# Performance work log

Measured on AMD Instinct MI355X. Metric: run time of the kernel, lower is better.

## Reference

```python
import jax, jax.numpy as jnp
import numpy as np

K = 7  # kernel_size
C, H, W = 32, 192, 192


def setup_inputs() -> dict:
    key = jax.random.key(0)
    k1, k2, k3, k4 = jax.random.split(key, 4)
    x = jax.random.normal(k1, (C, H, W, 2), dtype=jnp.float32)
    # per-pixel kernel: (1, 1, K^2, H, W); original inits to ones/K^2, randomize for testing
    weight1 = jax.random.normal(k2, (1, 1, K * K, H, W), dtype=jnp.float32) / (K * K)
    # 1x1 conv c->c: weight (C_out, C_in) and bias (C,)
    conv_w = jax.random.normal(k3, (C, C), dtype=jnp.float32) / np.sqrt(C).astype(np.float32)
    conv_b = jax.random.normal(k4, (C,), dtype=jnp.float32) * 0.01
    return {"x": x, "weight1": weight1, "conv_w": conv_w, "conv_b": conv_b}


def conv_pixelwise(x, kernel):
    # x: (n, c, h, w); kernel: (1, 1, K^2, h, w)
    # Equivalent to: pad, unfold(K), reshape (n,c,K^2,h,w), * kernel, sum over K^2.
    # Implemented as a fused shift-multiply-accumulate over the K^2 fixed taps
    p = K // 2
    n, c, h, w = x.shape
    xp = jnp.pad(x, ((0, 0), (0, 0), (p, p), (p, p)))
    out = jnp.zeros_like(x)
    for i in range(K):
        for j in range(K):
            # F.unfold ordering: row-major over the KxK window -> index i*K + j
            out = out + xp[:, :, i:i + h, j:j + w] * kernel[:, :, i * K + j]
    return out


def reference(x, weight1, conv_w, conv_b):
    # x: (c, h, w, 2) -> (2, c, h, w)
    xi = jnp.transpose(x, (3, 0, 1, 2))
    xi = conv_pixelwise(xi, weight1)
    # 1x1 conv over channels + bias
    xi = jnp.einsum('nchw,oc->nohw', xi, conv_w) + conv_b[None, :, None, None]
    # back to (c, h, w, 2)
    return jnp.transpose(xi, (1, 2, 3, 0))
```

## Files before the change

### kernel.cpp

```cpp
#include <hip/hip_runtime.h>

#define C 32
#define H 192
#define W 192
#define HW (H*W)
#define NPIX (HW*2)
#define KK 7

__global__ __launch_bounds__(256) void k1_mix(
    const float* __restrict__ x, const float* __restrict__ cw, float* __restrict__ z)
{
    __shared__ float wl[256];
    const int b  = blockIdx.x;
    const int l  = (b & 7) * 72 + (b >> 3);
    const int hwblk = l >> 2;
    const int ob    = (l & 3) * 8;
    const int tid   = threadIdx.x;

    wl[tid] = cw[(ob + (tid & 7)) * C + (tid >> 3)];
    __syncthreads();

    const int hw = hwblk * 256 + tid;
    const float2* x2 = reinterpret_cast<const float2*>(x);
    float2 xv[C];
#pragma unroll
    for (int c = 0; c < C; ++c) xv[c] = x2[(size_t)c * HW + hw];

    float acc[8][2];
#pragma unroll
    for (int oo = 0; oo < 8; ++oo) { acc[oo][0] = 0.f; acc[oo][1] = 0.f; }

#pragma unroll
    for (int c = 0; c < C; ++c) {
        const float4 wa = *reinterpret_cast<const float4*>(&wl[c * 8]);
        const float4 wb = *reinterpret_cast<const float4*>(&wl[c * 8 + 4]);
        const float wt[8] = { wa.x, wa.y, wa.z, wa.w, wb.x, wb.y, wb.z, wb.w };
#pragma unroll
        for (int oo = 0; oo < 8; ++oo) {
            acc[oo][0] += wt[oo] * xv[c].x;
            acc[oo][1] += wt[oo] * xv[c].y;
        }
    }

    float* zp = z + (size_t)hw * 64 + ob * 2;
#pragma unroll
    for (int q = 0; q < 4; ++q) {
        float4 r = make_float4(acc[2*q][0], acc[2*q][1], acc[2*q+1][0], acc[2*q+1][1]);
        *reinterpret_cast<float4*>(zp + 4 * q) = r;
    }
}

#define K2_BLOCKS 1152
__global__ __launch_bounds__(256) void k2_conv(
    const float* __restrict__ z, const float* __restrict__ w1,
    const float* __restrict__ cb, float* __restrict__ out)
{
    __shared__ float tr[4][8 * 66];

    const int b  = blockIdx.x;
    const int l  = (b & 7) * (K2_BLOCKS / 8) + (b >> 3);
    const int h  = l / 6;
    const int wq = l % 6;
    const int tid  = threadIdx.x;
    const int wv   = __builtin_amdgcn_readfirstlane(tid >> 6);
    const int lane = tid & 63;
    const int w0   = wq * 32 + wv * 8;

    float acc[8];
#pragma unroll
    for (int p = 0; p < 8; ++p) acc[p] = 0.f;

    const bool wedge = (w0 == 0) || (w0 == W - 8);

#pragma unroll
    for (int i = 0; i < KK; ++i) {
        const int yy = h + i - 3;
        if (yy < 0 || yy >= H) continue;

        float zw[14];
        if (!wedge) {
            const float* p = z + ((size_t)yy * W + (w0 - 3)) * 64 + lane;
#pragma unroll
            for (int k = 0; k < 14; ++k) zw[k] = p[k * 64];
        } else {
            const float* p = z + (size_t)yy * (W * 64) + lane;
#pragma unroll
            for (int k = 0; k < 14; ++k) {
                const int cc  = w0 - 3 + k;
                const int ccl = cc < 0 ? 0 : (cc > W - 1 ? W - 1 : cc);
                const float v = p[ccl * 64];
                zw[k] = (cc == ccl) ? v : 0.f;
            }
        }

        const float* wp = w1 + (size_t)i * KK * HW + (size_t)h * W + w0;
#pragma unroll
        for (int j = 0; j < KK; ++j) {
#pragma unroll
            for (int px = 0; px < 8; ++px)
                acc[px] += wp[(size_t)j * HW + px] * zw[j + px];
        }
    }

    const float bias = cb[lane >> 1];
    float* trw = &tr[wv][0];
#pragma unroll
    for (int p = 0; p < 8; ++p) trw[p * 66 + lane] = acc[p] + bias;
    __syncthreads();

    const int o = lane >> 1, half = lane & 1;
    float v8[8];
#pragma unroll
    for (int m = 0; m < 8; ++m) {
        const int f = half * 8 + m;
        v8[m] = trw[(f >> 1) * 66 + o * 2 + (f & 1)];
    }
    float* obase = out + (size_t)o * NPIX + ((size_t)h * W + w0) * 2 + half * 8;
    *reinterpret_cast<float4*>(obase)     = make_float4(v8[0], v8[1], v8[2], v8[3]);
    *reinterpret_cast<float4*>(obase + 4) = make_float4(v8[4], v8[5], v8[6], v8[7]);
}

extern "C" void kernel_launch(void* const* d_in, const int* in_sizes, int n_in,
                              void* d_out, int out_size, void* d_ws, size_t ws_size,
                              hipStream_t stream) {
    const float* x  = (const float*)d_in[0];
    const float* w1 = (const float*)d_in[1];
    const float* cw = (const float*)d_in[2];
    const float* cb = (const float*)d_in[3];
    float* z   = (float*)d_ws;
    float* out = (float*)d_out;

    hipLaunchKernelGGL(k1_mix, dim3(576), dim3(256), 0, stream, x, cw, z);
    hipLaunchKernelGGL(k2_conv, dim3(K2_BLOCKS), dim3(256), 0, stream, z, w1, cb, out);
}
```

Baseline: 23.89 us.

## Retile pixelwise conv to two rows per thread with float4 channel loads

The conv kernel now gives each lane 4 channel values (float4) for one pixel across two output rows. Each loaded z row feeds both output rows, which cuts z reloads, and the LDS transpose and barrier before the output store are gone. The mix kernel is split into 4 output channels per block with twice as many blocks, which lowers register pressure. The cost is narrower 8-byte output stores, per-lane weight loads with masked taps, and an extra boundary-specialized template path.

```diff
diff --git a/kernel.cpp b/kernel.cpp
--- a/kernel.cpp
+++ b/kernel.cpp
@@ -10,14 +10,14 @@
 __global__ __launch_bounds__(256) void k1_mix(
     const float* __restrict__ x, const float* __restrict__ cw, float* __restrict__ z)
 {
-    __shared__ float wl[256];
-    const int b  = blockIdx.x;
-    const int l  = (b & 7) * 72 + (b >> 3);
-    const int hwblk = l >> 2;
-    const int ob    = (l & 3) * 8;
+    __shared__ float wl[128];
+    const int b   = blockIdx.x;
+    const int xcd = b & 7, idx = b >> 3;
+    const int hwblk = xcd * 18 + (idx >> 3);
+    const int ob    = (idx & 7) * 4;
     const int tid   = threadIdx.x;
 
-    wl[tid] = cw[(ob + (tid & 7)) * C + (tid >> 3)];
+    if (tid < 128) wl[tid] = cw[(ob + (tid & 3)) * C + (tid >> 2)];
     __syncthreads();
 
     const int hw = hwblk * 256 + tid;
@@ -26,98 +26,109 @@
 #pragma unroll
     for (int c = 0; c < C; ++c) xv[c] = x2[(size_t)c * HW + hw];
 
-    float acc[8][2];
+    float acc[4][2];
 #pragma unroll
-    for (int oo = 0; oo < 8; ++oo) { acc[oo][0] = 0.f; acc[oo][1] = 0.f; }
+    for (int oo = 0; oo < 4; ++oo) { acc[oo][0] = 0.f; acc[oo][1] = 0.f; }
 
 #pragma unroll
     for (int c = 0; c < C; ++c) {
-        const float4 wa = *reinterpret_cast<const float4*>(&wl[c * 8]);
-        const float4 wb = *reinterpret_cast<const float4*>(&wl[c * 8 + 4]);
-        const float wt[8] = { wa.x, wa.y, wa.z, wa.w, wb.x, wb.y, wb.z, wb.w };
-#pragma unroll
-        for (int oo = 0; oo < 8; ++oo) {
-            acc[oo][0] += wt[oo] * xv[c].x;
-            acc[oo][1] += wt[oo] * xv[c].y;
-        }
+        const float4 wt = *reinterpret_cast<const float4*>(&wl[c * 4]);
+        acc[0][0] += wt.x * xv[c].x;  acc[0][1] += wt.x * xv[c].y;
+        acc[1][0] += wt.y * xv[c].x;  acc[1][1] += wt.y * xv[c].y;
+        acc[2][0] += wt.z * xv[c].x;  acc[2][1] += wt.z * xv[c].y;
+        acc[3][0] += wt.w * xv[c].x;  acc[3][1] += wt.w * xv[c].y;
     }
 
     float* zp = z + (size_t)hw * 64 + ob * 2;
+    *reinterpret_cast<float4*>(zp)     = make_float4(acc[0][0], acc[0][1], acc[1][0], acc[1][1]);
+    *reinterpret_cast<float4*>(zp + 4) = make_float4(acc[2][0], acc[2][1], acc[3][0], acc[3][1]);
+}
+
+#define K2_BLOCKS 1152
+
+template<bool HEDGE>
+__device__ __forceinline__ void k2_body(const float* __restrict__ z, const float* __restrict__ w1,
+                                        int h0, int w0, int px, int og, bool wedge, float acc[2][4])
+{
 #pragma unroll
-    for (int q = 0; q < 4; ++q) {
-        float4 r = make_float4(acc[2*q][0], acc[2*q][1], acc[2*q+1][0], acc[2*q+1][1]);
-        *reinterpret_cast<float4*>(zp + 4 * q) = r;
+    for (int s = 0; s < 8; ++s) {
+        const int yy = h0 - 3 + s;
+        if (HEDGE && (yy < 0 || yy >= H)) continue;
+
+        float4 zw[10];
+        if (!wedge) {
+            const float* p = z + ((size_t)yy * W + (w0 - 3)) * 64 + og * 4;
+#pragma unroll
+            for (int k = 0; k < 10; ++k)
+                zw[k] = *reinterpret_cast<const float4*>(p + (size_t)k * 64);
+        } else {
+            const float* p = z + (size_t)yy * (W * 64) + og * 4;
+#pragma unroll
+            for (int k = 0; k < 10; ++k) {
+                const int cc  = w0 - 3 + k;
+                const int ccl = cc < 0 ? 0 : (cc > W - 1 ? W - 1 : cc);
+                const float4 v = *reinterpret_cast<const float4*>(p + (size_t)ccl * 64);
+                zw[k] = (cc == ccl) ? v : make_float4(0.f, 0.f, 0.f, 0.f);
+            }
+        }
+
+#pragma unroll
+        for (int r = 0; r < 2; ++r) {
+            const int i = s - r;
+            if (i < 0 || i > 6) continue;
+            const float* wrow = w1 + (size_t)i * KK * HW + (size_t)(h0 + r) * W + w0 + px;
+#pragma unroll
+            for (int k = 0; k < 10; ++k) {
+                const int jj = k - px;
+                const bool v = (jj >= 0) && (jj <= 6);
+                const int jc = v ? jj : 0;
+                const float wt = v ? wrow[(size_t)jc * HW] : 0.f;
+                acc[r][0] += wt * zw[k].x;
+                acc[r][1] += wt * zw[k].y;
+                acc[r][2] += wt * zw[k].z;
+                acc[r][3] += wt * zw[k].w;
+            }
+        }
     }
 }
 
-#define K2_BLOCKS 1152
 __global__ __launch_bounds__(256) void k2_conv(
     const float* __restrict__ z, const float* __restrict__ w1,
     const float* __restrict__ cb, float* __restrict__ out)
 {
-    __shared__ float tr[4][8 * 66];
-
-    const int b  = blockIdx.x;
-    const int l  = (b & 7) * (K2_BLOCKS / 8) + (b >> 3);
-    const int h  = l / 6;
-    const int wq = l % 6;
+    const int b   = blockIdx.x;
+    const int xcd = b & 7, idx = b >> 3;
+    const int l   = xcd * (K2_BLOCKS / 8) + idx;
+    const int hp  = l / 12;
+    const int wq  = l % 12;
+    const int h0  = hp * 2;
     const int tid  = threadIdx.x;
     const int wv   = __builtin_amdgcn_readfirstlane(tid >> 6);
     const int lane = tid & 63;
-    const int w0   = wq * 32 + wv * 8;
+    const int px   = lane & 3;
+    const int og   = lane >> 2;
+    const int w0   = wq * 16 + wv * 4;
 
-    float acc[8];
+    float acc[2][4];
 #pragma unroll
-    for (int p = 0; p < 8; ++p) acc[p] = 0.f;
+    for (int r = 0; r < 2; ++r)
+#pragma unroll
+        for (int e = 0; e < 4; ++e) acc[r][e] = 0.f;
 
-    const bool wedge = (w0 == 0) || (w0 == W - 8);
+    const bool wedge = (w0 == 0) || (w0 == W - 4);
+    if (h0 >= 3 && h0 <= H - 6) k2_body<false>(z, w1, h0, w0, px, og, wedge, acc);
+    else                        k2_body<true >(z, w1, h0, w0, px, og, wedge, acc);
 
+    const float b0 = cb[og * 2];
+    const float b1 = cb[og * 2 + 1];
 #pragma unroll
-    for (int i = 0; i < KK; ++i) {
-        const int yy = h + i - 3;
-        if (yy < 0 || yy >= H) continue;
-
-        float zw[14];
-        if (!wedge) {
-            const float* p = z + ((size_t)yy * W + (w0 - 3)) * 64 + lane;
-#pragma unroll
-            for (int k = 0; k < 14; ++k) zw[k] = p[k * 64];
-        } else {
-            const float* p = z + (size_t)yy * (W * 64) + lane;
-#pragma unroll
-            for (int k = 0; k < 14; ++k) {
-                const int cc  = w0 - 3 + k;
-                const int ccl = cc < 0 ? 0 : (cc > W - 1 ? W - 1 : cc);
-                const float v = p[ccl * 64];
-                zw[k] = (cc == ccl) ? v : 0.f;
-            }
-        }
-
-        const float* wp = w1 + (size_t)i * KK * HW + (size_t)h * W + w0;
-#pragma unroll
-        for (int j = 0; j < KK; ++j) {
-#pragma unroll
-            for (int px = 0; px < 8; ++px)
-                acc[px] += wp[(size_t)j * HW + px] * zw[j + px];
-        }
+    for (int r = 0; r < 2; ++r) {
+        const size_t pofs = ((size_t)(h0 + r) * W + w0 + px) * 2;
+        float* p0 = out + (size_t)(og * 2)     * NPIX + pofs;
+        float* p1 = out + (size_t)(og * 2 + 1) * NPIX + pofs;
+        *reinterpret_cast<float2*>(p0) = make_float2(acc[r][0] + b0, acc[r][1] + b0);
+        *reinterpret_cast<float2*>(p1) = make_float2(acc[r][2] + b1, acc[r][3] + b1);
     }
-
-    const float bias = cb[lane >> 1];
-    float* trw = &tr[wv][0];
-#pragma unroll
-    for (int p = 0; p < 8; ++p) trw[p * 66 + lane] = acc[p] + bias;
-    __syncthreads();
-
-    const int o = lane >> 1, half = lane & 1;
-    float v8[8];
-#pragma unroll
-    for (int m = 0; m < 8; ++m) {
-        const int f = half * 8 + m;
-        v8[m] = trw[(f >> 1) * 66 + o * 2 + (f & 1)];
-    }
-    float* obase = out + (size_t)o * NPIX + ((size_t)h * W + w0) * 2 + half * 8;
-    *reinterpret_cast<float4*>(obase)     = make_float4(v8[0], v8[1], v8[2], v8[3]);
-    *reinterpret_cast<float4*>(obase + 4) = make_float4(v8[4], v8[5], v8[6], v8[7]);
 }
 
 extern "C" void kernel_launch(void* const* d_in, const int* in_sizes, int n_in,
@@ -130,6 +141,6 @@
     float* z   = (float*)d_ws;
     float* out = (float*)d_out;
 
-    hipLaunchKernelGGL(k1_mix, dim3(576), dim3(256), 0, stream, x, cw, z);
+    hipLaunchKernelGGL(k1_mix, dim3(1152), dim3(256), 0, stream, x, cw, z);
     hipLaunchKernelGGL(k2_conv, dim3(K2_BLOCKS), dim3(256), 0, stream, z, w1, cb, out);
 }
```

Result: slower. 59.33 us (+148.4%).
